# Kernel tuning notes

Hardware: AMD Instinct MI355X
Metric: run time of the kernel (lower is better)

The kernel has to match this reference:

```python
import jax, jax.numpy as jnp
import numpy as np

INPUT_DIM = 1024
OUTPUT_DIM = 1024
DEGREE = 8
N_TOKENS = 8192


def setup_inputs() -> dict:
    key = jax.random.key(0)
    k1, k2 = jax.random.split(key)
    x = jax.random.normal(k1, (N_TOKENS, INPUT_DIM), dtype=jnp.float32)
    # xavier_normal_ with gain = 1/(input_dim*(degree+1)) over fan dims (output_dim, degree+1)
    fan_in, fan_out = OUTPUT_DIM, DEGREE + 1  # torch treats dim0/dim1 as fans; scale is tiny anyway
    gain = 1.0 / (INPUT_DIM * (DEGREE + 1))
    std = gain * np.sqrt(2.0 / (INPUT_DIM + OUTPUT_DIM))
    cheby_coeffs = std * jax.random.normal(k2, (INPUT_DIM, OUTPUT_DIM, DEGREE + 1), dtype=jnp.float32)
    return {"x": x, "cheby_coeffs": cheby_coeffs}


def reference(x, cheby_coeffs):
    # x: (..., input_dim) -> y: (..., output_dim)
    degree_p1 = cheby_coeffs.shape[-1]
    theta = jnp.arccos(jnp.tanh(x))                      # (..., i)
    arange = jnp.arange(degree_p1, dtype=x.dtype)        # (d,)
    basis = jnp.cos(theta[..., None] * arange)           # (..., i, d) Chebyshev T_d(tanh(x))
    y = jnp.einsum('...id,iod->...o', basis, cheby_coeffs)
    return y
```

## Files before the change

### kernel.cpp

```cpp
#include <hip/hip_runtime.h>


typedef __bf16 bf16;
typedef __bf16 bf16x8 __attribute__((ext_vector_type(8)));
typedef float f32x2 __attribute__((ext_vector_type(2)));
typedef float f32x4 __attribute__((ext_vector_type(4)));
typedef float f32x16 __attribute__((ext_vector_type(16)));

#define MFMA __builtin_amdgcn_mfma_f32_32x32x16_bf16

__device__ __forceinline__ void g2lds16(const void* g, void* l) {
  __builtin_amdgcn_global_load_lds(
      (const __attribute__((address_space(1))) unsigned int*)g,
      (__attribute__((address_space(3))) unsigned int*)l, 16, 0, 0);
}

__device__ __forceinline__ float fast_tanh(float a) {
  float e = __expf(a + a);
  return 1.f - 2.f * __builtin_amdgcn_rcpf(e + 1.f);
}

__global__ __launch_bounds__(256)
void cheby_prep6(const float* __restrict__ x, const float* __restrict__ C,
                 bf16* __restrict__ B, float* __restrict__ bias_p,
                 float* __restrict__ th2) {
  const int bid = blockIdx.x, tid = threadIdx.x;
  if (bid < 1024) {
    __shared__ float xs[64][129];
    const int r0 = (bid >> 3) * 64, c0 = (bid & 7) * 128;
    #pragma unroll
    for (int it = 0; it < 8; ++it) {
      const int e = tid + it * 256;
      const int rr = e >> 5, c4 = (e & 31) * 4;
      f32x4 v = *(const f32x4*)(x + (size_t)(r0 + rr) * 1024 + c0 + c4);
      xs[rr][c4 + 0] = v.x; xs[rr][c4 + 1] = v.y;
      xs[rr][c4 + 2] = v.z; xs[rr][c4 + 3] = v.w;
    }
    __syncthreads();
    const int row = tid & 63, kq = tid >> 6;
    const int mb = r0 >> 8, rowp = (r0 & 255) + row;
    const int kt0 = c0 >> 3;
    float* outp = th2 + (size_t)mb * 128 * 2048;
    #pragma unroll
    for (int kk = 0; kk < 4; ++kk) {
      const int kt = kq * 4 + kk;
      #pragma unroll
      for (int li = 0; li < 8; ++li) {
        float z = fast_tanh(xs[row][kt * 8 + li]);
        const int pos = (li & 1) * 4 + (li >> 1);
        outp[((size_t)(kt0 + kt) * 8 + pos) * 256 + rowp] = z;
      }
    }
    return;
  }
  const int b2 = bid - 1024;
  __shared__ float tile[32][292];
  const int i0 = (b2 >> 5) * 32, o0 = (b2 & 31) * 32;
  {
    const int r = tid >> 3, seg = tid & 7;
    const float* src = C + (size_t)(i0 + r) * 9216 + (size_t)o0 * 9 + seg * 36;
    float* dst = &tile[r][seg * 36];
    #pragma unroll
    for (int v = 0; v < 9; ++v) *(f32x4*)(dst + v * 4) = *(const f32x4*)(src + v * 4);
  }
  __syncthreads();
  #pragma unroll
  for (int j = 0; j < 4; ++j) {
    int e = tid + 256 * j;
    int il = e >> 5, ol = e & 31;
    int i = i0 + il, o = o0 + ol;
    bf16x8 v;
    #pragma unroll
    for (int d = 0; d < 8; ++d) v[d] = (bf16)tile[il][ol * 9 + 1 + d];
    const int cc = i & 7;
    size_t tnum = (size_t)(o >> 7) * 128 + (i >> 3);
    const int widx = (((cc >> 1) * 4 + ((o & 127) >> 5)) * 2 + (cc & 1)) * 32 + (o & 31);
    *(bf16x8*)(B + tnum * 8192 + widx * 8) = v;
  }
  if (tid < 32) {
    float s = 0.f;
    #pragma unroll
    for (int i = 0; i < 32; ++i) s += tile[i][tid * 9];
    bias_p[(size_t)(b2 >> 5) * 1024 + o0 + tid] = s;
  }
}

__global__ __launch_bounds__(512, 2)
void cheby_gemm7(const float* __restrict__ th2, const bf16* __restrict__ B,
                 const float* __restrict__ bias_p, float* __restrict__ out) {
  __shared__ bf16 ring[3][12288];
  const int tid = threadIdx.x;
  const int lane = tid & 63, w = tid >> 6;
  const int wm = w >> 1, wn = w & 1;
  const int bid = blockIdx.x;
  const int wgid = (bid & 7) * 32 + (bid >> 3);
  const int mb2 = wgid >> 3, nb = wgid & 7;

  const int ml = lane & 31, h = lane >> 5;
  const int bBase = wn * 1024 + h * 256 + ml * 8;
  const int row0 = wm * 64;
  const int sOff = h * 1024 + row0 + ml;

  const bf16*  bG = B   + (size_t)nb * 1048576 + tid * 8;
  const float* tG = th2 + (size_t)mb2 * 262144 + tid * 4;

  f32x16 acc[2][2];
  #pragma unroll
  for (int a = 0; a < 2; ++a)
    #pragma unroll
    for (int b = 0; b < 2; ++b)
      #pragma unroll
      for (int r = 0; r < 16; ++r) acc[a][b][r] = 0.f;

  auto issue3 = [&](int t, int p) {
    g2lds16(bG + (size_t)t * 8192,        &ring[p][tid * 8]);
    g2lds16(bG + (size_t)t * 8192 + 4096, &ring[p][4096 + tid * 8]);
    g2lds16(tG + (size_t)t * 2048,        &ring[p][8192 + tid * 8]);
  };

  issue3(0, 0); issue3(1, 1);
  asm volatile("s_waitcnt vmcnt(3)" ::: "memory");
  __builtin_amdgcn_s_barrier();

  auto step = [&](int t, int pC, int pN) {
    if (t + 2 < 128) issue3(t + 2, pN);
    const bf16* ra = &ring[pC][0];
    const float* seedL = (const float*)(ra + 8192);
    bf16x8 bfr[2][4], afr[2][4];
    #pragma unroll
    for (int ks = 0; ks < 4; ++ks) {
      bfr[0][ks] = *(const bf16x8*)(ra + bBase + ks * 2048);
      bfr[1][ks] = *(const bf16x8*)(ra + bBase + ks * 2048 + 512);
    }
    #pragma unroll
    for (int ks = 0; ks < 4; ++ks) {
      f32x2 tv = { seedL[sOff + ks * 256], seedL[sOff + ks * 256 + 32] };
      f32x2 t2 = tv + tv;
      f32x2 prev = {1.f, 1.f}, cur = tv;
      #pragma unroll
      for (int j = 0; j < 8; ++j) {
        afr[0][ks][j] = (bf16)cur.x;
        afr[1][ks][j] = (bf16)cur.y;
        f32x2 nx = t2 * cur - prev;
        prev = cur; cur = nx;
      }
    }
    __builtin_amdgcn_s_setprio(1);
    #pragma unroll
    for (int ks = 0; ks < 4; ++ks) {
      acc[0][0] = MFMA(afr[0][ks], bfr[0][ks], acc[0][0], 0, 0, 0);
      acc[0][1] = MFMA(afr[0][ks], bfr[1][ks], acc[0][1], 0, 0, 0);
      acc[1][0] = MFMA(afr[1][ks], bfr[0][ks], acc[1][0], 0, 0, 0);
      acc[1][1] = MFMA(afr[1][ks], bfr[1][ks], acc[1][1], 0, 0, 0);
    }
    __builtin_amdgcn_s_setprio(0);
    asm volatile("s_waitcnt lgkmcnt(0)" ::: "memory");
    if (t <= 125) asm volatile("s_waitcnt vmcnt(3)" ::: "memory");
    else          asm volatile("s_waitcnt vmcnt(0)" ::: "memory");
    __builtin_amdgcn_s_barrier();
  };

  #pragma unroll 1
  for (int t3 = 0; t3 < 126; t3 += 3) {
    step(t3,     0, 2);
    step(t3 + 1, 1, 0);
    step(t3 + 2, 2, 1);
  }
  step(126, 0, 2);
  step(127, 1, 0);

  const int c0 = nb * 128 + wn * 64 + ml;
  float bv0 = 0.f, bv1 = 0.f;
  #pragma unroll
  for (int p = 0; p < 32; ++p) {
    bv0 += bias_p[(size_t)p * 1024 + c0];
    bv1 += bias_p[(size_t)p * 1024 + c0 + 32];
  }
  const int r0 = mb2 * 256 + wm * 64;
  #pragma unroll
  for (int mt = 0; mt < 2; ++mt)
    #pragma unroll
    for (int r = 0; r < 16; ++r) {
      int row = r0 + mt * 32 + (r & 3) + 8 * (r >> 2) + 4 * h;
      float* po = out + (size_t)row * 1024 + c0;
      po[0]  = acc[mt][0][r] + bv0;
      po[32] = acc[mt][1][r] + bv1;
    }
}

__global__ __launch_bounds__(256)
void cheby_naive(const float* __restrict__ x, const float* __restrict__ C,
                 float* __restrict__ out) {
  const int t = blockIdx.x, tid = threadIdx.x;
  float acc[4] = {0.f, 0.f, 0.f, 0.f};
  for (int i = 0; i < 1024; ++i) {
    float th = tanhf(x[(size_t)t * 1024 + i]);
    float T[9]; T[0] = 1.f; T[1] = th;
    #pragma unroll
    for (int d = 2; d < 9; ++d) T[d] = 2.f * th * T[d - 1] - T[d - 2];
    #pragma unroll
    for (int j = 0; j < 4; ++j) {
      const float* cp = &C[((size_t)i * 1024 + tid + j * 256) * 9];
      float s = 0.f;
      #pragma unroll
      for (int d = 0; d < 9; ++d) s += T[d] * cp[d];
      acc[j] += s;
    }
  }
  #pragma unroll
  for (int j = 0; j < 4; ++j) out[(size_t)t * 1024 + tid + j * 256] = acc[j];
}

extern "C" void kernel_launch(void* const* d_in, const int* in_sizes, int n_in,
                              void* d_out, int out_size, void* d_ws, size_t ws_size,
                              hipStream_t stream) {
  (void)in_sizes; (void)n_in; (void)out_size;
  const float* x = (const float*)d_in[0];
  const float* C = (const float*)d_in[1];
  float* out = (float*)d_out;

  const size_t b_bytes  = (size_t)8 * 128 * 8192 * 2;
  const size_t bp_bytes = (size_t)32 * 1024 * 4;
  const size_t th_bytes = (size_t)32 * 128 * 8 * 256 * 4;

  if (ws_size >= b_bytes + bp_bytes + th_bytes) {
    bf16*  B      = (bf16*)d_ws;
    float* bias_p = (float*)((char*)d_ws + b_bytes);
    float* th2    = (float*)((char*)d_ws + b_bytes + bp_bytes);
    cheby_prep6<<<2048, 256, 0, stream>>>(x, C, B, bias_p, th2);
    cheby_gemm7<<<256, 512, 0, stream>>>(th2, B, bias_p, out);
  } else {
    cheby_naive<<<8192, 256, 0, stream>>>(x, C, out);
  }
}
```

Before: 245.1 us.

## Split GEMM K dimension in two with partial buffers and a combine kernel

Splits the reduction over input features into two halves so the GEMM launches 512 workgroups instead of 256, each writing fp32 partial results to a workspace buffer. A new combine kernel adds the two partials plus a precomputed bias. The prep kernel is split into a coefficient-packing kernel and a tanh/bias-reduction kernel. The aim is better CU occupancy on the GEMM, at the cost of an extra 64MB of partial-sum writes and reads plus two more kernel launches.

```diff
diff --git a/kernel.cpp b/kernel.cpp
--- a/kernel.cpp
+++ b/kernel.cpp
@@ -21,39 +21,9 @@
 }
 
 __global__ __launch_bounds__(256)
-void cheby_prep6(const float* __restrict__ x, const float* __restrict__ C,
-                 bf16* __restrict__ B, float* __restrict__ bias_p,
-                 float* __restrict__ th2) {
-  const int bid = blockIdx.x, tid = threadIdx.x;
-  if (bid < 1024) {
-    __shared__ float xs[64][129];
-    const int r0 = (bid >> 3) * 64, c0 = (bid & 7) * 128;
-    #pragma unroll
-    for (int it = 0; it < 8; ++it) {
-      const int e = tid + it * 256;
-      const int rr = e >> 5, c4 = (e & 31) * 4;
-      f32x4 v = *(const f32x4*)(x + (size_t)(r0 + rr) * 1024 + c0 + c4);
-      xs[rr][c4 + 0] = v.x; xs[rr][c4 + 1] = v.y;
-      xs[rr][c4 + 2] = v.z; xs[rr][c4 + 3] = v.w;
-    }
-    __syncthreads();
-    const int row = tid & 63, kq = tid >> 6;
-    const int mb = r0 >> 8, rowp = (r0 & 255) + row;
-    const int kt0 = c0 >> 3;
-    float* outp = th2 + (size_t)mb * 128 * 2048;
-    #pragma unroll
-    for (int kk = 0; kk < 4; ++kk) {
-      const int kt = kq * 4 + kk;
-      #pragma unroll
-      for (int li = 0; li < 8; ++li) {
-        float z = fast_tanh(xs[row][kt * 8 + li]);
-        const int pos = (li & 1) * 4 + (li >> 1);
-        outp[((size_t)(kt0 + kt) * 8 + pos) * 256 + rowp] = z;
-      }
-    }
-    return;
-  }
-  const int b2 = bid - 1024;
+void cheby_prepB(const float* __restrict__ C, bf16* __restrict__ B,
+                 float* __restrict__ bias_p) {
+  const int b2 = blockIdx.x, tid = threadIdx.x;
   __shared__ float tile[32][292];
   const int i0 = (b2 >> 5) * 32, o0 = (b2 & 31) * 32;
   {
@@ -85,24 +55,64 @@
   }
 }
 
-__global__ __launch_bounds__(512, 2)
-void cheby_gemm7(const float* __restrict__ th2, const bf16* __restrict__ B,
-                 const float* __restrict__ bias_p, float* __restrict__ out) {
+__global__ __launch_bounds__(256)
+void cheby_prepT(const float* __restrict__ x, const float* __restrict__ bias_p,
+                 float* __restrict__ th2, float* __restrict__ bias) {
+  const int bid = blockIdx.x, tid = threadIdx.x;
+  if (bid >= 1024) {
+    const int col = (bid - 1024) * 256 + tid;
+    float s = 0.f;
+    #pragma unroll
+    for (int p = 0; p < 32; ++p) s += bias_p[(size_t)p * 1024 + col];
+    bias[col] = s;
+    return;
+  }
+  __shared__ float xs[64][129];
+  const int r0 = (bid >> 3) * 64, c0 = (bid & 7) * 128;
+  #pragma unroll
+  for (int it = 0; it < 8; ++it) {
+    const int e = tid + it * 256;
+    const int rr = e >> 5, c4 = (e & 31) * 4;
+    f32x4 v = *(const f32x4*)(x + (size_t)(r0 + rr) * 1024 + c0 + c4);
+    xs[rr][c4 + 0] = v.x; xs[rr][c4 + 1] = v.y;
+    xs[rr][c4 + 2] = v.z; xs[rr][c4 + 3] = v.w;
+  }
+  __syncthreads();
+  const int row = tid & 63, kq = tid >> 6;
+  const int mb = r0 >> 8, rowp = (r0 & 255) + row;
+  const int kt0 = c0 >> 3;
+  float* outp = th2 + (size_t)mb * 128 * 2048;
+  #pragma unroll
+  for (int kk = 0; kk < 4; ++kk) {
+    const int kt = kq * 4 + kk;
+    #pragma unroll
+    for (int li = 0; li < 8; ++li) {
+      float z = fast_tanh(xs[row][kt * 8 + li]);
+      const int pos = (li & 1) * 4 + (li >> 1);
+      outp[((size_t)(kt0 + kt) * 8 + pos) * 256 + rowp] = z;
+    }
+  }
+}
+
+__global__ __launch_bounds__(512, 4)
+void cheby_gemm8(const float* __restrict__ th2, const bf16* __restrict__ B,
+                 float* __restrict__ part) {
   __shared__ bf16 ring[3][12288];
   const int tid = threadIdx.x;
   const int lane = tid & 63, w = tid >> 6;
   const int wm = w >> 1, wn = w & 1;
   const int bid = blockIdx.x;
-  const int wgid = (bid & 7) * 32 + (bid >> 3);
-  const int mb2 = wgid >> 3, nb = wgid & 7;
+  const int wgid = (bid & 7) * 64 + (bid >> 3);
+  const int tile = wgid >> 1, kh = wgid & 1;
+  const int mb2 = tile >> 3, nb = tile & 7;
 
   const int ml = lane & 31, h = lane >> 5;
   const int bBase = wn * 1024 + h * 256 + ml * 8;
   const int row0 = wm * 64;
   const int sOff = h * 1024 + row0 + ml;
 
-  const bf16*  bG = B   + (size_t)nb * 1048576 + tid * 8;
-  const float* tG = th2 + (size_t)mb2 * 262144 + tid * 4;
+  const bf16*  bG = B   + (size_t)nb * 1048576 + (size_t)kh * 524288 + tid * 8;
+  const float* tG = th2 + (size_t)mb2 * 262144 + (size_t)kh * 131072 + tid * 4;
 
   f32x16 acc[2][2];
   #pragma unroll
@@ -123,7 +133,7 @@
   __builtin_amdgcn_s_barrier();
 
   auto step = [&](int t, int pC, int pN) {
-    if (t + 2 < 128) issue3(t + 2, pN);
+    if (t + 2 < 64) issue3(t + 2, pN);
     const bf16* ra = &ring[pC][0];
     const float* seedL = (const float*)(ra + 8192);
     bf16x8 bfr[2][4], afr[2][4];
@@ -155,37 +165,42 @@
     }
     __builtin_amdgcn_s_setprio(0);
     asm volatile("s_waitcnt lgkmcnt(0)" ::: "memory");
-    if (t <= 125) asm volatile("s_waitcnt vmcnt(3)" ::: "memory");
-    else          asm volatile("s_waitcnt vmcnt(0)" ::: "memory");
+    if (t <= 61) asm volatile("s_waitcnt vmcnt(3)" ::: "memory");
+    else         asm volatile("s_waitcnt vmcnt(0)" ::: "memory");
     __builtin_amdgcn_s_barrier();
   };
 
   #pragma unroll 1
-  for (int t3 = 0; t3 < 126; t3 += 3) {
+  for (int t3 = 0; t3 < 63; t3 += 3) {
     step(t3,     0, 2);
     step(t3 + 1, 1, 0);
     step(t3 + 2, 2, 1);
   }
-  step(126, 0, 2);
-  step(127, 1, 0);
+  step(63, 0, 2);
 
   const int c0 = nb * 128 + wn * 64 + ml;
-  float bv0 = 0.f, bv1 = 0.f;
-  #pragma unroll
-  for (int p = 0; p < 32; ++p) {
-    bv0 += bias_p[(size_t)p * 1024 + c0];
-    bv1 += bias_p[(size_t)p * 1024 + c0 + 32];
-  }
   const int r0 = mb2 * 256 + wm * 64;
+  float* pb = part + (size_t)kh * 8388608;
   #pragma unroll
   for (int mt = 0; mt < 2; ++mt)
     #pragma unroll
     for (int r = 0; r < 16; ++r) {
       int row = r0 + mt * 32 + (r & 3) + 8 * (r >> 2) + 4 * h;
-      float* po = out + (size_t)row * 1024 + c0;
-      po[0]  = acc[mt][0][r] + bv0;
-      po[32] = acc[mt][1][r] + bv1;
-    }
+      float* po = pb + (size_t)row * 1024 + c0;
+      po[0]  = acc[mt][0][r];
+      po[32] = acc[mt][1][r];
+    }
+}
+
+__global__ __launch_bounds__(256)
+void cheby_combine(const float* __restrict__ part, const float* __restrict__ bias,
+                   float* __restrict__ out) {
+  const size_t e = ((size_t)blockIdx.x * 256 + threadIdx.x) * 4;
+  f32x4 p0 = *(const f32x4*)(part + e);
+  f32x4 p1 = *(const f32x4*)(part + 8388608 + e);
+  f32x4 b  = *(const f32x4*)(bias + (e & 1023));
+  f32x4 r  = p0 + p1 + b;
+  *(f32x4*)(out + e) = r;
 }
 
 __global__ __launch_bounds__(256)
@@ -219,16 +234,23 @@
   const float* C = (const float*)d_in[1];
   float* out = (float*)d_out;
 
-  const size_t b_bytes  = (size_t)8 * 128 * 8192 * 2;
-  const size_t bp_bytes = (size_t)32 * 1024 * 4;
-  const size_t th_bytes = (size_t)32 * 128 * 8 * 256 * 4;
-
-  if (ws_size >= b_bytes + bp_bytes + th_bytes) {
-    bf16*  B      = (bf16*)d_ws;
-    float* bias_p = (float*)((char*)d_ws + b_bytes);
-    float* th2    = (float*)((char*)d_ws + b_bytes + bp_bytes);
-    cheby_prep6<<<2048, 256, 0, stream>>>(x, C, B, bias_p, th2);
-    cheby_gemm7<<<256, 512, 0, stream>>>(th2, B, bias_p, out);
+  const size_t b_bytes    = (size_t)8 * 128 * 8192 * 2;
+  const size_t bp_bytes   = (size_t)32 * 1024 * 4;
+  const size_t bias_bytes = (size_t)1024 * 4 + 3072;
+  const size_t th_bytes   = (size_t)32 * 128 * 8 * 256 * 4;
+  const size_t part_bytes = (size_t)2 * 8192 * 1024 * 4;
+
+  if (ws_size >= b_bytes + bp_bytes + bias_bytes + th_bytes + part_bytes) {
+    char* p = (char*)d_ws;
+    bf16*  B      = (bf16*)p;                          p += b_bytes;
+    float* bias_p = (float*)p;                         p += bp_bytes;
+    float* bias   = (float*)p;                         p += bias_bytes;
+    float* th2    = (float*)p;                         p += th_bytes;
+    float* part   = (float*)p;
+    cheby_prepB<<<1024, 256, 0, stream>>>(C, B, bias_p);
+    cheby_prepT<<<1028, 256, 0, stream>>>(x, bias_p, th2, bias);
+    cheby_gemm8<<<512, 512, 0, stream>>>(th2, B, part);
+    cheby_combine<<<8192, 256, 0, stream>>>(part, bias, out);
   } else {
     cheby_naive<<<8192, 256, 0, stream>>>(x, C, out);
   }
```

Result: slower. 557.7 us (+127.5%).

## Halve GEMM M-tile to 128 rows with 4-wave blocks and split prep kernel

Applied to the files above, without the earlier changes.

The GEMM now uses 256-thread workgroups covering a 128x128 output tile instead of 512 threads covering 256x128, and launches 512 workgroups instead of 256. The tanh layout in the workspace is re-tiled to match, and the fused prep kernel is split into separate B-conversion and tanh kernels. Smaller tiles raise the workgroup count and may improve CU occupancy and load balance across the 256 CUs. In exchange, B tiles are reused across fewer rows, so global and L2 traffic for B roughly doubles, and the extra kernel launch adds overhead.

```diff
diff --git a/kernel.cpp b/kernel.cpp
--- a/kernel.cpp
+++ b/kernel.cpp
@@ -21,39 +21,9 @@
 }
 
 __global__ __launch_bounds__(256)
-void cheby_prep6(const float* __restrict__ x, const float* __restrict__ C,
-                 bf16* __restrict__ B, float* __restrict__ bias_p,
-                 float* __restrict__ th2) {
-  const int bid = blockIdx.x, tid = threadIdx.x;
-  if (bid < 1024) {
-    __shared__ float xs[64][129];
-    const int r0 = (bid >> 3) * 64, c0 = (bid & 7) * 128;
-    #pragma unroll
-    for (int it = 0; it < 8; ++it) {
-      const int e = tid + it * 256;
-      const int rr = e >> 5, c4 = (e & 31) * 4;
-      f32x4 v = *(const f32x4*)(x + (size_t)(r0 + rr) * 1024 + c0 + c4);
-      xs[rr][c4 + 0] = v.x; xs[rr][c4 + 1] = v.y;
-      xs[rr][c4 + 2] = v.z; xs[rr][c4 + 3] = v.w;
-    }
-    __syncthreads();
-    const int row = tid & 63, kq = tid >> 6;
-    const int mb = r0 >> 8, rowp = (r0 & 255) + row;
-    const int kt0 = c0 >> 3;
-    float* outp = th2 + (size_t)mb * 128 * 2048;
-    #pragma unroll
-    for (int kk = 0; kk < 4; ++kk) {
-      const int kt = kq * 4 + kk;
-      #pragma unroll
-      for (int li = 0; li < 8; ++li) {
-        float z = fast_tanh(xs[row][kt * 8 + li]);
-        const int pos = (li & 1) * 4 + (li >> 1);
-        outp[((size_t)(kt0 + kt) * 8 + pos) * 256 + rowp] = z;
-      }
-    }
-    return;
-  }
-  const int b2 = bid - 1024;
+void cheby_prepB(const float* __restrict__ C, bf16* __restrict__ B,
+                 float* __restrict__ bias_p) {
+  const int b2 = blockIdx.x, tid = threadIdx.x;
   __shared__ float tile[32][292];
   const int i0 = (b2 >> 5) * 32, o0 = (b2 & 31) * 32;
   {
@@ -85,24 +55,53 @@
   }
 }
 
-__global__ __launch_bounds__(512, 2)
-void cheby_gemm7(const float* __restrict__ th2, const bf16* __restrict__ B,
+__global__ __launch_bounds__(256)
+void cheby_prepT(const float* __restrict__ x, float* __restrict__ th2) {
+  const int bid = blockIdx.x, tid = threadIdx.x;
+  __shared__ float xs[64][129];
+  const int r0 = (bid >> 3) * 64, c0 = (bid & 7) * 128;
+  #pragma unroll
+  for (int it = 0; it < 8; ++it) {
+    const int e = tid + it * 256;
+    const int rr = e >> 5, c4 = (e & 31) * 4;
+    f32x4 v = *(const f32x4*)(x + (size_t)(r0 + rr) * 1024 + c0 + c4);
+    xs[rr][c4 + 0] = v.x; xs[rr][c4 + 1] = v.y;
+    xs[rr][c4 + 2] = v.z; xs[rr][c4 + 3] = v.w;
+  }
+  __syncthreads();
+  const int row = tid & 63, kq = tid >> 6;
+  const int mt = r0 >> 7, rowp = (r0 & 127) + row;
+  const int kt0 = c0 >> 3;
+  float* outp = th2 + (size_t)mt * 131072;
+  #pragma unroll
+  for (int kk = 0; kk < 4; ++kk) {
+    const int kt = kq * 4 + kk;
+    #pragma unroll
+    for (int li = 0; li < 8; ++li) {
+      float z = fast_tanh(xs[row][kt * 8 + li]);
+      const int pos = (li & 1) * 4 + (li >> 1);
+      outp[(size_t)(kt0 + kt) * 1024 + pos * 128 + rowp] = z;
+    }
+  }
+}
+
+__global__ __launch_bounds__(256, 2)
+void cheby_gemm9(const float* __restrict__ th2, const bf16* __restrict__ B,
                  const float* __restrict__ bias_p, float* __restrict__ out) {
-  __shared__ bf16 ring[3][12288];
+  __shared__ bf16 ring[3][10240];
   const int tid = threadIdx.x;
   const int lane = tid & 63, w = tid >> 6;
   const int wm = w >> 1, wn = w & 1;
   const int bid = blockIdx.x;
-  const int wgid = (bid & 7) * 32 + (bid >> 3);
-  const int mb2 = wgid >> 3, nb = wgid & 7;
+  const int wgid = (bid & 7) * 64 + (bid >> 3);
+  const int mt = wgid >> 3, nb = wgid & 7;
 
   const int ml = lane & 31, h = lane >> 5;
   const int bBase = wn * 1024 + h * 256 + ml * 8;
-  const int row0 = wm * 64;
-  const int sOff = h * 1024 + row0 + ml;
+  const int sBase = h * 512 + wm * 64 + ml;
 
   const bf16*  bG = B   + (size_t)nb * 1048576 + tid * 8;
-  const float* tG = th2 + (size_t)mb2 * 262144 + tid * 4;
+  const float* tG = th2 + (size_t)mt * 131072 + tid * 4;
 
   f32x16 acc[2][2];
   #pragma unroll
@@ -112,18 +111,19 @@
       #pragma unroll
       for (int r = 0; r < 16; ++r) acc[a][b][r] = 0.f;
 
-  auto issue3 = [&](int t, int p) {
-    g2lds16(bG + (size_t)t * 8192,        &ring[p][tid * 8]);
-    g2lds16(bG + (size_t)t * 8192 + 4096, &ring[p][4096 + tid * 8]);
-    g2lds16(tG + (size_t)t * 2048,        &ring[p][8192 + tid * 8]);
+  auto issue5 = [&](int t, int p) {
+    #pragma unroll
+    for (int c = 0; c < 4; ++c)
+      g2lds16(bG + (size_t)t * 8192 + c * 2048, &ring[p][c * 2048 + tid * 8]);
+    g2lds16(tG + (size_t)t * 1024, &ring[p][8192 + tid * 8]);
   };
 
-  issue3(0, 0); issue3(1, 1);
-  asm volatile("s_waitcnt vmcnt(3)" ::: "memory");
+  issue5(0, 0); issue5(1, 1);
+  asm volatile("s_waitcnt vmcnt(5)" ::: "memory");
   __builtin_amdgcn_s_barrier();
 
   auto step = [&](int t, int pC, int pN) {
-    if (t + 2 < 128) issue3(t + 2, pN);
+    if (t + 2 < 128) issue5(t + 2, pN);
     const bf16* ra = &ring[pC][0];
     const float* seedL = (const float*)(ra + 8192);
     bf16x8 bfr[2][4], afr[2][4];
@@ -134,7 +134,7 @@
     }
     #pragma unroll
     for (int ks = 0; ks < 4; ++ks) {
-      f32x2 tv = { seedL[sOff + ks * 256], seedL[sOff + ks * 256 + 32] };
+      f32x2 tv = { seedL[sBase + ks * 128], seedL[sBase + ks * 128 + 32] };
       f32x2 t2 = tv + tv;
       f32x2 prev = {1.f, 1.f}, cur = tv;
       #pragma unroll
@@ -155,7 +155,7 @@
     }
     __builtin_amdgcn_s_setprio(0);
     asm volatile("s_waitcnt lgkmcnt(0)" ::: "memory");
-    if (t <= 125) asm volatile("s_waitcnt vmcnt(3)" ::: "memory");
+    if (t <= 125) asm volatile("s_waitcnt vmcnt(5)" ::: "memory");
     else          asm volatile("s_waitcnt vmcnt(0)" ::: "memory");
     __builtin_amdgcn_s_barrier();
   };
@@ -176,15 +176,15 @@
     bv0 += bias_p[(size_t)p * 1024 + c0];
     bv1 += bias_p[(size_t)p * 1024 + c0 + 32];
   }
-  const int r0 = mb2 * 256 + wm * 64;
-  #pragma unroll
-  for (int mt = 0; mt < 2; ++mt)
+  const int r0 = mt * 128 + wm * 64;
+  #pragma unroll
+  for (int mtt = 0; mtt < 2; ++mtt)
     #pragma unroll
     for (int r = 0; r < 16; ++r) {
-      int row = r0 + mt * 32 + (r & 3) + 8 * (r >> 2) + 4 * h;
+      int row = r0 + mtt * 32 + (r & 3) + 8 * (r >> 2) + 4 * h;
       float* po = out + (size_t)row * 1024 + c0;
-      po[0]  = acc[mt][0][r] + bv0;
-      po[32] = acc[mt][1][r] + bv1;
+      po[0]  = acc[mtt][0][r] + bv0;
+      po[32] = acc[mtt][1][r] + bv1;
     }
 }
 
@@ -221,14 +221,15 @@
 
   const size_t b_bytes  = (size_t)8 * 128 * 8192 * 2;
   const size_t bp_bytes = (size_t)32 * 1024 * 4;
-  const size_t th_bytes = (size_t)32 * 128 * 8 * 256 * 4;
+  const size_t th_bytes = (size_t)64 * 128 * 1024 * 4;
 
   if (ws_size >= b_bytes + bp_bytes + th_bytes) {
     bf16*  B      = (bf16*)d_ws;
     float* bias_p = (float*)((char*)d_ws + b_bytes);
     float* th2    = (float*)((char*)d_ws + b_bytes + bp_bytes);
-    cheby_prep6<<<2048, 256, 0, stream>>>(x, C, B, bias_p, th2);
-    cheby_gemm7<<<256, 512, 0, stream>>>(th2, B, bias_p, out);
+    cheby_prepB<<<1024, 256, 0, stream>>>(C, B, bias_p);
+    cheby_prepT<<<1024, 256, 0, stream>>>(x, th2);
+    cheby_gemm9<<<512, 256, 0, stream>>>(th2, B, bias_p, out);
   } else {
     cheby_naive<<<8192, 256, 0, stream>>>(x, C, out);
   }
```

Measured after the change: 255.4 us. 1.04x slower.
